# Optimization experiments

Hardware: AMD Instinct MI355X
Metric: run time of the kernel (lower is better)

## Reference

```python
import jax, jax.numpy as jnp
import numpy as np

B, DIN, H, DOUT = 4096, 2048, 4096, 2048


def setup_inputs() -> dict:
    key = jax.random.key(0)
    ks = jax.random.split(key, 17)
    x = jax.random.normal(ks[0], (B, DIN), dtype=jnp.float32)
    W0 = jax.random.randint(ks[1], (H, DIN), -127, 128, dtype=jnp.int32)
    b0 = jax.random.randint(ks[2], (H,), -127, 128, dtype=jnp.int32)
    W2 = jax.random.randint(ks[3], (H, H), -127, 128, dtype=jnp.int32)
    b2 = jax.random.randint(ks[4], (H,), -127, 128, dtype=jnp.int32)
    W4 = jax.random.randint(ks[5], (DOUT, H), -127, 128, dtype=jnp.int32)
    b4 = jax.random.randint(ks[6], (DOUT,), -127, 128, dtype=jnp.int32)
    # amax scalars: positive calibration ranges in [0.5, 2.0)
    amaxes = [jax.random.uniform(ks[7 + i], (), jnp.float32, 0.5, 2.0) for i in range(9)]
    (a0_in, a0_w, a0_b, a2_in, a2_w, a2_b, a4_in, a4_w, a4_b) = amaxes
    return {"x": x, "W0": W0, "b0": b0, "W2": W2, "b2": b2, "W4": W4, "b4": b4,
            "a0_in": a0_in, "a0_w": a0_w, "a0_b": a0_b,
            "a2_in": a2_in, "a2_w": a2_w, "a2_b": a2_b,
            "a4_in": a4_in, "a4_w": a4_w, "a4_b": a4_b}


def _quant(x, amax):
    # torch: clamp(round(x * 127/amax), -127, 127).int()
    scale = 127.0 / amax
    return jnp.clip(jnp.round(x * scale), -127.0, 127.0).astype(jnp.int32)


def _layer(x, W, b, a_in, a_w, a_b):
    xq = _quant(x, a_in)                                      # [B, in] int32
    acc = jnp.matmul(xq, W.T, preferred_element_type=jnp.int32)  # [B, out] int32
    y = acc.astype(jnp.float32) * (a_w * a_in / (127.0 ** 2))    # double dequant
    return y + b.astype(jnp.float32) * (a_b / 127.0)             # single dequant bias


def reference(x, W0, b0, W2, b2, W4, b4,
              a0_in, a0_w, a0_b, a2_in, a2_w, a2_b, a4_in, a4_w, a4_b):
    x = x.reshape(x.shape[0], -1)
    x = _layer(x, W0, b0, a0_in, a0_w, a0_b)
    x = jax.nn.relu(x)
    x = _layer(x, W2, b2, a2_in, a2_w, a2_b)
    x = jax.nn.relu(x)
    x = _layer(x, W4, b4, a4_in, a4_w, a4_b)
    return x
```

## Files before the change

kernel.cpp:

```cpp
#include <hip/hip_runtime.h>

using i32x4 = __attribute__((ext_vector_type(4))) int;

#define DEVI static __device__ __forceinline__

DEVI void gload_lds16(const void* g, void* l) {
  __builtin_amdgcn_global_load_lds(
      (const __attribute__((address_space(1))) void*)g,
      (__attribute__((address_space(3))) void*)l, 16, 0, 0);
}

#define FENCE() asm volatile("" ::: "memory")
#define BARX()                        \
  do {                                \
    FENCE();                          \
    __builtin_amdgcn_s_barrier();     \
    FENCE();                          \
  } while (0)
#define LGKM0() asm volatile("s_waitcnt lgkmcnt(0)" ::: "memory")
#define VMC(n) asm volatile("s_waitcnt vmcnt(" #n ")" ::: "memory")
#define PRIO1() __builtin_amdgcn_s_setprio(1)
#define PRIO0() __builtin_amdgcn_s_setprio(0)

__global__ void __launch_bounds__(256) pack_w_kernel(const int* __restrict__ w,
                                                     signed char* __restrict__ o,
                                                     int n4) {
  int stride = gridDim.x * blockDim.x;
  for (int i = blockIdx.x * blockDim.x + threadIdx.x; i < n4; i += stride) {
    int4 v = reinterpret_cast<const int4*>(w)[i];
    char4 c;
    c.x = (signed char)v.x;
    c.y = (signed char)v.y;
    c.z = (signed char)v.z;
    c.w = (signed char)v.w;
    reinterpret_cast<char4*>(o)[i] = c;
  }
}

__global__ void __launch_bounds__(256) quant_x_kernel(const float* __restrict__ x,
                                                      signed char* __restrict__ o,
                                                      const float* __restrict__ amax,
                                                      int n4) {
  const float s = 127.0f / amax[0];
  int stride = gridDim.x * blockDim.x;
  for (int i = blockIdx.x * blockDim.x + threadIdx.x; i < n4; i += stride) {
    float4 v = reinterpret_cast<const float4*>(x)[i];
    char4 c;
    float q;
    q = fminf(fmaxf(rintf(__fmul_rn(v.x, s)), -127.0f), 127.0f); c.x = (signed char)(int)q;
    q = fminf(fmaxf(rintf(__fmul_rn(v.y, s)), -127.0f), 127.0f); c.y = (signed char)(int)q;
    q = fminf(fmaxf(rintf(__fmul_rn(v.z, s)), -127.0f), 127.0f); c.z = (signed char)(int)q;
    q = fminf(fmaxf(rintf(__fmul_rn(v.w, s)), -127.0f), 127.0f); c.w = (signed char)(int)q;
    reinterpret_cast<char4*>(o)[i] = c;
  }
}


#define STAGE(buf, kt)                                                          \
  do {                                                                          \
    const int k0_ = (kt) * 128 + scol;                                          \
    _Pragma("unroll") for (int j = 0; j < NN; ++j)                              \
        gload_lds16(Wb + (size_t)(j * 64 + srow) * K + k0_,                     \
                    &lds[buf][ABYTES + j * 8192 + tid * 16]);                   \
    gload_lds16(Ab + (size_t)(srow) * K + k0_, &lds[buf][tid * 16]);            \
    gload_lds16(Ab + (size_t)(128 + srow) * K + k0_, &lds[buf][16384 + tid * 16]); \
    gload_lds16(Ab + (size_t)(64 + srow) * K + k0_, &lds[buf][8192 + tid * 16]);   \
    gload_lds16(Ab + (size_t)(192 + srow) * K + k0_, &lds[buf][24576 + tid * 16]); \
  } while (0)

#define AF_(buf, m, h) \
  (*(const i32x4*)&lds[buf][(wrl + (m)*16 + ro) * 128 + ((h) ? cS1 : cS0)])
#define BF_(buf, n, h) \
  (*(const i32x4*)&lds[buf][ABYTES + (wcl + (n)*16 + ro) * 128 + ((h) ? cS1 : cS0)])

#define READ_AF(buf, m0)       \
  do {                         \
    af[0][0] = AF_(buf, m0, 0);      \
    af[0][1] = AF_(buf, m0, 1);      \
    af[1][0] = AF_(buf, (m0) + 1, 0); \
    af[1][1] = AF_(buf, (m0) + 1, 1); \
  } while (0)

#define READ_BF(buf)                               \
  do {                                             \
    _Pragma("unroll") for (int n = 0; n < NN; ++n) { \
      bf[n][0] = BF_(buf, n, 0);                   \
      bf[n][1] = BF_(buf, n, 1);                   \
    }                                              \
  } while (0)

#define MFMA_PAIR(mp)                                                                        \
  do {                                                                                       \
    _Pragma("unroll") for (int n = 0; n < NN; ++n) {                                         \
      acc[2 * (mp)][n] =                                                                     \
          __builtin_amdgcn_mfma_i32_16x16x64_i8(af[0][0], bf[n][0], acc[2 * (mp)][n], 0, 0, 0); \
      acc[2 * (mp)][n] =                                                                     \
          __builtin_amdgcn_mfma_i32_16x16x64_i8(af[0][1], bf[n][1], acc[2 * (mp)][n], 0, 0, 0); \
      acc[2 * (mp) + 1][n] = __builtin_amdgcn_mfma_i32_16x16x64_i8(af[1][0], bf[n][0],       \
                                                                   acc[2 * (mp) + 1][n], 0, 0, 0); \
      acc[2 * (mp) + 1][n] = __builtin_amdgcn_mfma_i32_16x16x64_i8(af[1][1], bf[n][1],       \
                                                                   acc[2 * (mp) + 1][n], 0, 0, 0); \
    }                                                                                        \
  } while (0)

#define TILE(buf, t)                                                     \
  do {                                                                   \
    READ_BF(buf);                                                        \
    READ_AF(buf, 0);                                                     \
    BARX(); LGKM0(); PRIO1(); MFMA_PAIR(0); PRIO0(); BARX();             \
    READ_AF(buf, 2);                                                     \
    BARX(); LGKM0(); PRIO1(); MFMA_PAIR(1); PRIO0(); VMC(0); BARX();     \
    if ((t) + 1 < nt) STAGE(1 - (buf), (t) + 1);                         \
    READ_AF(buf, 4);                                                     \
    BARX(); LGKM0(); PRIO1(); MFMA_PAIR(2); PRIO0(); BARX();             \
    READ_AF(buf, 6);                                                     \
    BARX(); LGKM0(); PRIO1(); MFMA_PAIR(3); PRIO0(); VMC(2); BARX();     \
  } while (0)

template <int BN, int OUT_I8>
__global__ __launch_bounds__(512, 2) void gemm8_kernel(
    const signed char* __restrict__ A, const signed char* __restrict__ W,
    const int* __restrict__ bias, void* __restrict__ out, int M, int N, int K,
    const float* __restrict__ p_ain, const float* __restrict__ p_aw,
    const float* __restrict__ p_ab, const float* __restrict__ p_anext) {
  static_assert(BN == 256 || BN == 128, "");
  constexpr int NN = BN / 64;
  constexpr int ABYTES = 256 * 128;
  __shared__ signed char lds[2][ABYTES + BN * 128];

  const int tid = threadIdx.x;
  const int lane = tid & 63;
  const int wave = tid >> 6;
  const int wrl = (wave >> 2) * 128;
  const int wcl = (wave & 3) * (BN / 4);
  const int tileM = blockIdx.y * 256;
  const int tileN = blockIdx.x * BN;

  const signed char* Ab = A + (size_t)tileM * K;
  const signed char* Wb = W + (size_t)tileN * K;

  const int srow = tid >> 3;
  const int scol = ((tid & 7) ^ (srow & 7)) * 16;

  const int ro = lane & 15;
  const int kg = lane >> 4;
  const int cS0 = ((kg ^ (ro & 7)) << 4);
  const int cS1 = (((4 + kg) ^ (ro & 7)) << 4);

  const int nt = K >> 7;

  i32x4 acc[8][NN] = {};
  i32x4 af[2][2], bf[NN][2];

  STAGE(0, 0);
  VMC(2);
  BARX();

  for (int t = 0; t < nt; t += 2) {
    TILE(0, t);
    TILE(1, t + 1);
  }

  const float s1 = __fmul_rn(p_aw[0], p_ain[0]) / 16129.0f;
  const float s2 = p_ab[0] / 127.0f;
  float qs = 0.0f;
  if (OUT_I8) qs = 127.0f / p_anext[0];

#pragma unroll
  for (int m = 0; m < 8; ++m) {
#pragma unroll
    for (int n = 0; n < NN; ++n) {
      const int col = tileN + wcl + n * 16 + ro;
      const int row0 = tileM + wrl + m * 16 + kg * 4;
      const float bv = __fmul_rn((float)bias[col], s2);
#pragma unroll
      for (int i = 0; i < 4; ++i) {
        float y = __fadd_rn(__fmul_rn((float)acc[m][n][i], s1), bv);
        if (OUT_I8) {
          float rl = fmaxf(y, 0.0f);
          float q = fminf(rintf(__fmul_rn(rl, qs)), 127.0f);
          ((signed char*)out)[(size_t)(row0 + i) * N + col] = (signed char)(int)q;
        } else {
          ((float*)out)[(size_t)(row0 + i) * N + col] = y;
        }
      }
    }
  }
}

extern "C" void kernel_launch(void* const* d_in, const int* in_sizes, int n_in,
                              void* d_out, int out_size, void* d_ws, size_t ws_size,
                              hipStream_t stream) {
  const float* x = (const float*)d_in[0];
  const int* W0 = (const int*)d_in[1];
  const int* b0 = (const int*)d_in[2];
  const int* W2 = (const int*)d_in[3];
  const int* b2 = (const int*)d_in[4];
  const int* W4 = (const int*)d_in[5];
  const int* b4 = (const int*)d_in[6];
  const float* a0_in = (const float*)d_in[7];
  const float* a0_w = (const float*)d_in[8];
  const float* a0_b = (const float*)d_in[9];
  const float* a2_in = (const float*)d_in[10];
  const float* a2_w = (const float*)d_in[11];
  const float* a2_b = (const float*)d_in[12];
  const float* a4_in = (const float*)d_in[13];
  const float* a4_w = (const float*)d_in[14];
  const float* a4_b = (const float*)d_in[15];

  constexpr int Bb = 4096, DIN = 2048, H = 4096, DOUT = 2048;
  constexpr size_t MB = 1u << 20;

  char* ws = (char*)d_ws;
  signed char* xq0 = (signed char*)(ws);
  signed char* xq2 = (signed char*)(ws);
  signed char* W0q = (signed char*)(ws + 8 * MB);
  signed char* W2q = (signed char*)(ws + 16 * MB);
  signed char* W4q = (signed char*)(ws + 32 * MB);
  signed char* xq1 = (signed char*)(ws + 40 * MB);

  pack_w_kernel<<<2048, 256, 0, stream>>>(W0, W0q, H * DIN / 4);
  pack_w_kernel<<<2048, 256, 0, stream>>>(W2, W2q, H * H / 4);
  pack_w_kernel<<<2048, 256, 0, stream>>>(W4, W4q, DOUT * H / 4);
  quant_x_kernel<<<2048, 256, 0, stream>>>(x, xq0, a0_in, Bb * DIN / 4);

  gemm8_kernel<256, 1><<<dim3(H / 256, Bb / 256), 512, 0, stream>>>(
      xq0, W0q, b0, xq1, Bb, H, DIN, a0_in, a0_w, a0_b, a2_in);
  gemm8_kernel<256, 1><<<dim3(H / 256, Bb / 256), 512, 0, stream>>>(
      xq1, W2q, b2, xq2, Bb, H, H, a2_in, a2_w, a2_b, a4_in);
  gemm8_kernel<128, 0><<<dim3(DOUT / 128, Bb / 256), 512, 0, stream>>>(
      xq2, W4q, b4, d_out, Bb, DOUT, H, a4_in, a4_w, a4_b, a4_in);
}
```

Baseline: 185.9 us.

## Double-buffer A fragments and split global staging across MFMA phases

Restructures the int8 GEMM main loop so A-fragment LDS reads are double-buffered (afA/afB), with the next phase's reads issued before the current MFMA block. Global-to-LDS staging of the next K tile is split into B and A parts and spread across the phases. Waits are relaxed to partial lgkmcnt/vmcnt counts, and sched_barrier keeps the ordering fixed. The aim is to hide LDS and global latency behind MFMA work and drop redundant barriers. In exchange it adds register pressure and relies on the exact waitcnt counts being correct.

```diff
diff --git a/kernel.cpp b/kernel.cpp
--- a/kernel.cpp
+++ b/kernel.cpp
@@ -10,15 +10,21 @@
       (__attribute__((address_space(3))) void*)l, 16, 0, 0);
 }
 
+template <int N> DEVI void vmcnt_n() {
+  asm volatile("s_waitcnt vmcnt(%0)" ::"n"(N) : "memory");
+}
+template <int N> DEVI void lgkm_n() {
+  asm volatile("s_waitcnt lgkmcnt(%0)" ::"n"(N) : "memory");
+}
+
 #define FENCE() asm volatile("" ::: "memory")
-#define BARX()                        \
-  do {                                \
-    FENCE();                          \
-    __builtin_amdgcn_s_barrier();     \
-    FENCE();                          \
-  } while (0)
-#define LGKM0() asm volatile("s_waitcnt lgkmcnt(0)" ::: "memory")
-#define VMC(n) asm volatile("s_waitcnt vmcnt(" #n ")" ::: "memory")
+#define BARX()                    \
+  do {                            \
+    FENCE();                      \
+    __builtin_amdgcn_s_barrier(); \
+    FENCE();                      \
+  } while (0)
+#define SCHB() __builtin_amdgcn_sched_barrier(0)
 #define PRIO1() __builtin_amdgcn_s_setprio(1)
 #define PRIO0() __builtin_amdgcn_s_setprio(0)
 
@@ -56,65 +62,98 @@
 }
 
 
-#define STAGE(buf, kt)                                                          \
-  do {                                                                          \
-    const int k0_ = (kt) * 128 + scol;                                          \
-    _Pragma("unroll") for (int j = 0; j < NN; ++j)                              \
-        gload_lds16(Wb + (size_t)(j * 64 + srow) * K + k0_,                     \
-                    &lds[buf][ABYTES + j * 8192 + tid * 16]);                   \
-    gload_lds16(Ab + (size_t)(srow) * K + k0_, &lds[buf][tid * 16]);            \
-    gload_lds16(Ab + (size_t)(128 + srow) * K + k0_, &lds[buf][16384 + tid * 16]); \
-    gload_lds16(Ab + (size_t)(64 + srow) * K + k0_, &lds[buf][8192 + tid * 16]);   \
-    gload_lds16(Ab + (size_t)(192 + srow) * K + k0_, &lds[buf][24576 + tid * 16]); \
-  } while (0)
-
-#define AF_(buf, m, h) \
-  (*(const i32x4*)&lds[buf][(wrl + (m)*16 + ro) * 128 + ((h) ? cS1 : cS0)])
-#define BF_(buf, n, h) \
-  (*(const i32x4*)&lds[buf][ABYTES + (wcl + (n)*16 + ro) * 128 + ((h) ? cS1 : cS0)])
-
-#define READ_AF(buf, m0)       \
-  do {                         \
-    af[0][0] = AF_(buf, m0, 0);      \
-    af[0][1] = AF_(buf, m0, 1);      \
-    af[1][0] = AF_(buf, (m0) + 1, 0); \
-    af[1][1] = AF_(buf, (m0) + 1, 1); \
-  } while (0)
-
-#define READ_BF(buf)                               \
+#define GB(b, j, k0_)                                           \
+  gload_lds16(Wb + (size_t)((j)*64 + srow) * K + (k0_),         \
+              &lds[b][ABYTES + (j)*8192 + tid * 16])
+#define GA(b, r0, k0_)                                          \
+  gload_lds16(Ab + (size_t)((r0) + srow) * K + (k0_),           \
+              &lds[b][(r0)*128 + tid * 16])
+
+#define STG_B(b, kt)                               \
   do {                                             \
+    const int k0_ = (kt)*128 + scol;               \
+    _Pragma("unroll") for (int j = 0; j < NN; ++j) GB(b, j, k0_); \
+  } while (0)
+#define STG_A(b, kt)                 \
+  do {                               \
+    const int k0_ = (kt)*128 + scol; \
+    GA(b, 0, k0_);                   \
+    GA(b, 128, k0_);                 \
+    GA(b, 64, k0_);                  \
+    GA(b, 192, k0_);                 \
+  } while (0)
+
+#define AF_(b, m, h) \
+  (*(const i32x4*)&lds[b][(wrl + (m)*16 + ro) * 128 + ((h) ? cS1 : cS0)])
+#define BF_(b, n, h) \
+  (*(const i32x4*)&lds[b][ABYTES + (wcl + (n)*16 + ro) * 128 + ((h) ? cS1 : cS0)])
+
+#define RD_AF(dst, b, m0)          \
+  do {                             \
+    dst[0][0] = AF_(b, m0, 0);     \
+    dst[0][1] = AF_(b, m0, 1);     \
+    dst[1][0] = AF_(b, (m0) + 1, 0); \
+    dst[1][1] = AF_(b, (m0) + 1, 1); \
+  } while (0)
+
+#define READ_BF(b)                                   \
+  do {                                               \
     _Pragma("unroll") for (int n = 0; n < NN; ++n) { \
-      bf[n][0] = BF_(buf, n, 0);                   \
-      bf[n][1] = BF_(buf, n, 1);                   \
-    }                                              \
-  } while (0)
-
-#define MFMA_PAIR(mp)                                                                        \
-  do {                                                                                       \
-    _Pragma("unroll") for (int n = 0; n < NN; ++n) {                                         \
-      acc[2 * (mp)][n] =                                                                     \
+      bf[n][0] = BF_(b, n, 0);                       \
+      bf[n][1] = BF_(b, n, 1);                       \
+    }                                                \
+  } while (0)
+
+#define MFMA_P(mp, af)                                                                     \
+  do {                                                                                     \
+    _Pragma("unroll") for (int n = 0; n < NN; ++n) {                                       \
+      acc[2 * (mp)][n] =                                                                   \
           __builtin_amdgcn_mfma_i32_16x16x64_i8(af[0][0], bf[n][0], acc[2 * (mp)][n], 0, 0, 0); \
-      acc[2 * (mp)][n] =                                                                     \
+      acc[2 * (mp)][n] =                                                                   \
           __builtin_amdgcn_mfma_i32_16x16x64_i8(af[0][1], bf[n][1], acc[2 * (mp)][n], 0, 0, 0); \
-      acc[2 * (mp) + 1][n] = __builtin_amdgcn_mfma_i32_16x16x64_i8(af[1][0], bf[n][0],       \
-                                                                   acc[2 * (mp) + 1][n], 0, 0, 0); \
-      acc[2 * (mp) + 1][n] = __builtin_amdgcn_mfma_i32_16x16x64_i8(af[1][1], bf[n][1],       \
-                                                                   acc[2 * (mp) + 1][n], 0, 0, 0); \
-    }                                                                                        \
-  } while (0)
-
-#define TILE(buf, t)                                                     \
-  do {                                                                   \
-    READ_BF(buf);                                                        \
-    READ_AF(buf, 0);                                                     \
-    BARX(); LGKM0(); PRIO1(); MFMA_PAIR(0); PRIO0(); BARX();             \
-    READ_AF(buf, 2);                                                     \
-    BARX(); LGKM0(); PRIO1(); MFMA_PAIR(1); PRIO0(); VMC(0); BARX();     \
-    if ((t) + 1 < nt) STAGE(1 - (buf), (t) + 1);                         \
-    READ_AF(buf, 4);                                                     \
-    BARX(); LGKM0(); PRIO1(); MFMA_PAIR(2); PRIO0(); BARX();             \
-    READ_AF(buf, 6);                                                     \
-    BARX(); LGKM0(); PRIO1(); MFMA_PAIR(3); PRIO0(); VMC(2); BARX();     \
+      acc[2 * (mp) + 1][n] = __builtin_amdgcn_mfma_i32_16x16x64_i8(                        \
+          af[1][0], bf[n][0], acc[2 * (mp) + 1][n], 0, 0, 0);                              \
+      acc[2 * (mp) + 1][n] = __builtin_amdgcn_mfma_i32_16x16x64_i8(                        \
+          af[1][1], bf[n][1], acc[2 * (mp) + 1][n], 0, 0, 0);                              \
+    }                                                                                      \
+  } while (0)
+
+#define TILE_STEADY(b, t)                       \
+  do {                                          \
+    READ_BF(b);                                 \
+    RD_AF(afB, b, 2);                           \
+    STG_B(1 - (b), (t) + 1);                    \
+    vmcnt_n<VM0>();                             \
+    BARX(); lgkm_n<4>(); SCHB();                \
+    PRIO1(); MFMA_P(0, afA); PRIO0();           \
+    RD_AF(afA, b, 4);                           \
+    STG_A(1 - (b), (t) + 1);                    \
+    BARX(); lgkm_n<4>(); SCHB();                \
+    PRIO1(); MFMA_P(1, afB); PRIO0();           \
+    RD_AF(afB, b, 6);                           \
+    vmcnt_n<2>();                               \
+    BARX(); lgkm_n<4>(); SCHB();                \
+    PRIO1(); MFMA_P(2, afA); PRIO0();           \
+    RD_AF(afA, 1 - (b), 0);                     \
+    BARX(); lgkm_n<4>(); SCHB();                \
+    PRIO1(); MFMA_P(3, afB); PRIO0();           \
+  } while (0)
+
+#define TILE_LAST(b)                            \
+  do {                                          \
+    READ_BF(b);                                 \
+    RD_AF(afB, b, 2);                           \
+    vmcnt_n<0>();                               \
+    BARX(); lgkm_n<4>(); SCHB();                \
+    PRIO1(); MFMA_P(0, afA); PRIO0();           \
+    RD_AF(afA, b, 4);                           \
+    BARX(); lgkm_n<4>(); SCHB();                \
+    PRIO1(); MFMA_P(1, afB); PRIO0();           \
+    RD_AF(afB, b, 6);                           \
+    BARX(); lgkm_n<4>(); SCHB();                \
+    PRIO1(); MFMA_P(2, afA); PRIO0();           \
+    BARX(); lgkm_n<0>(); SCHB();                \
+    PRIO1(); MFMA_P(3, afB); PRIO0();           \
   } while (0)
 
 template <int BN, int OUT_I8>
@@ -125,6 +164,7 @@
     const float* __restrict__ p_ab, const float* __restrict__ p_anext) {
   static_assert(BN == 256 || BN == 128, "");
   constexpr int NN = BN / 64;
+  constexpr int VM0 = (NN == 4) ? 4 : 2;
   constexpr int ABYTES = 256 * 128;
   __shared__ signed char lds[2][ABYTES + BN * 128];
 
@@ -150,16 +190,20 @@
   const int nt = K >> 7;
 
   i32x4 acc[8][NN] = {};
-  i32x4 af[2][2], bf[NN][2];
-
-  STAGE(0, 0);
-  VMC(2);
+  i32x4 afA[2][2], afB[2][2], bf[NN][2];
+
+  STG_B(0, 0);
+  STG_A(0, 0);
+  vmcnt_n<2>();
   BARX();
-
-  for (int t = 0; t < nt; t += 2) {
-    TILE(0, t);
-    TILE(1, t + 1);
-  }
+  RD_AF(afA, 0, 0);
+
+  for (int t = 0; t < nt - 2; t += 2) {
+    TILE_STEADY(0, t);
+    TILE_STEADY(1, t + 1);
+  }
+  TILE_STEADY(0, nt - 2);
+  TILE_LAST(1);
 
   const float s1 = __fmul_rn(p_aw[0], p_ain[0]) / 16129.0f;
   const float s2 = p_ab[0] / 127.0f;
```

Measured after the change: 171.5 us. 7.8% less time.
